# Kernel optimization log

Measured on AMD Instinct MI355X. Metric: run time of the kernel, lower is better.

The kernel has to match this reference:

```python
import jax, jax.numpy as jnp
import numpy as np

N = 100000      # nodes
E = 1000000     # edges
IN = 64         # in_dim
TD = 64         # time_dim
OUT = 64        # out_dim
H = 4           # num_heads
HD = OUT // H   # head_dim = 16


def setup_inputs() -> dict:
    key = jax.random.key(0)
    ks = jax.random.split(key, 12)
    g = lambda k, shp, s: (jax.random.normal(k, shp, jnp.float32) * s)
    return {
        "x": g(ks[0], (N, IN), 1.0),
        "time_features": g(ks[1], (N, TD), 1.0),
        "edge_index": jax.random.randint(ks[2], (2, E), 0, N, dtype=jnp.int32),
        # nn.Linear weights stored as [in, out] (already transposed)
        "q_w": g(ks[3], (IN + TD, OUT), 0.05), "q_b": g(ks[4], (OUT,), 0.05),
        "k_w": g(ks[5], (IN + TD, OUT), 0.05), "k_b": g(ks[6], (OUT,), 0.05),
        "v_w": g(ks[7], (IN, OUT), 0.05),      "v_b": g(ks[8], (OUT,), 0.05),
        "o_w": g(ks[9], (OUT, OUT), 0.05),     "o_b": g(ks[10], (OUT,), 0.05),
    }


def reference(x, time_features, edge_index, q_w, q_b, k_w, k_b, v_w, v_b, o_w, o_b):
    xt = jnp.concatenate([x, time_features], axis=-1)            # [N, IN+TD]
    Q = (xt @ q_w + q_b).reshape(N, H, HD)
    K = (xt @ k_w + k_b).reshape(N, H, HD)
    V = (x @ v_w + v_b).reshape(N, H, HD)
    src, dst = edge_index[0], edge_index[1]
    # edge-gather QK dot-product: [E, H]
    scores = jnp.sum(Q[dst] * K[src], axis=-1) / np.float32(np.sqrt(HD))
    # per-destination (segment) softmax over edges, numerically stable two-pass
    seg_max = jax.ops.segment_max(scores, dst, num_segments=N)   # [N, H]
    e = jnp.exp(scores - seg_max[dst])                           # [E, H]
    seg_sum = jax.ops.segment_sum(e, dst, num_segments=N)        # [N, H]
    attn = e / seg_sum[dst]                                      # [E, H]
    # weighted scatter-add of values
    messages = attn[..., None] * V[src]                          # [E, H, HD]
    out = jax.ops.segment_sum(messages, dst, num_segments=N)     # [N, H, HD]
    out = out.reshape(N, OUT)
    return out @ o_w + o_b
```

## Files before the change

### kernel.cpp

```cpp
#include <hip/hip_runtime.h>
#include <hip/hip_fp16.h>
#include <math.h>

#define N_NODES 100000
#define N_EDGES 1000000
#define QKV_BLOCKS ((N_NODES + 63) / 64)
#define FILL_BLOCKS ((N_EDGES + 255) / 256)
#define PREP_BLOCKS 96
#define HEAD_INT4 ((N_NODES * 8) / 4)
#define ZERO_BLOCKS ((HEAD_INT4 + 255) / 256)
#define AGG_BLOCKS (N_NODES / 16)

typedef __attribute__((ext_vector_type(8))) _Float16 f16x8;
typedef __attribute__((ext_vector_type(4))) float    f32x4;

__global__ __launch_bounds__(256) void prep_zero_kernel(
    const float* __restrict__ qw, const float* __restrict__ kw,
    const float* __restrict__ vw, const float* __restrict__ ow,
    _Float16* __restrict__ WqT, _Float16* __restrict__ WkT,
    _Float16* __restrict__ WvT, _Float16* __restrict__ WoT,
    int* __restrict__ head)
{
    if (blockIdx.x < PREP_BLOCKS) {
        const int idx = blockIdx.x * 256 + threadIdx.x;
        if (idx < 8192) {
            const int c = idx >> 7, k = idx & 127;
            WqT[idx] = (_Float16)qw[k * 64 + c];
        } else if (idx < 16384) {
            const int i = idx - 8192, c = i >> 7, k = i & 127;
            WkT[i] = (_Float16)kw[k * 64 + c];
        } else if (idx < 20480) {
            const int i = idx - 16384, c = i >> 6, k = i & 63;
            WvT[i] = (_Float16)vw[k * 64 + c];
        } else {
            const int i = idx - 20480, c = i >> 6, k = i & 63;
            WoT[i] = (_Float16)ow[k * 64 + c];
        }
    } else {
        const int idx = (blockIdx.x - PREP_BLOCKS) * 256 + threadIdx.x;
        if (idx < HEAD_INT4)
            ((int4*)head)[idx] = make_int4(-1, -1, -1, -1);
    }
}

__global__ __launch_bounds__(256) void fill_qkv_kernel(
    const int* __restrict__ src, const int* __restrict__ dst,
    int* __restrict__ head, int2* __restrict__ next2,
    const float* __restrict__ x, const float* __restrict__ tf,
    const _Float16* __restrict__ WqT, const _Float16* __restrict__ WkT,
    const _Float16* __restrict__ WvT,
    const float* __restrict__ qb, const float* __restrict__ kb,
    const float* __restrict__ vb,
    _Float16* __restrict__ Qh, _Float16* __restrict__ Kh,
    _Float16* __restrict__ Vh)
{
    __shared__ _Float16 xt[64][128];
    const int t = threadIdx.x;

    if (blockIdx.x >= QKV_BLOCKS) {
        const int e = (blockIdx.x - QKV_BLOCKS) * 256 + t;
        if (e < N_EDGES) {
            const int d  = dst[e];
            const int sv = src[e];
            const int old = atomicExch(&head[(size_t)d * 8 + (e & 7)], e);
            next2[e] = make_int2(old, sv);
        }
        return;
    }

    const int base = blockIdx.x * 64;

    {
        const int j = t & 15;
        #pragma unroll
        for (int i = 0; i < 4; ++i) {
            const int r = (t >> 4) + 16 * i;
            int node = base + r;
            if (node >= N_NODES) node = N_NODES - 1;
            const float* p = (j < 8) ? (x  + (size_t)node * 64 + 8 * j)
                                     : (tf + (size_t)node * 64 + 8 * (j - 8));
            const float4 lo = ((const float4*)p)[0];
            const float4 hi = ((const float4*)p)[1];
            f16x8 h = { (_Float16)lo.x, (_Float16)lo.y, (_Float16)lo.z,
                        (_Float16)lo.w, (_Float16)hi.x, (_Float16)hi.y,
                        (_Float16)hi.z, (_Float16)hi.w };
            const int js = j ^ (r & 15);
            *(f16x8*)&xt[r][js * 8] = h;
        }
    }

    const int wave = t >> 6;
    const int lane = t & 63;
    const int lrow = lane & 15;
    const int lgrp = lane >> 4;
    const int cw   = wave * 16;

    f16x8 bq[4], bk[4], bv[2];
    const float biasq = qb[cw + lrow];
    const float biask = kb[cw + lrow];
    const float biasv = vb[cw + lrow];
    {
        const size_t rq = (size_t)(cw + lrow) * 128 + lgrp * 8;
        #pragma unroll
        for (int kt = 0; kt < 4; ++kt) {
            bq[kt] = *(const f16x8*)&WqT[rq + kt * 32];
            bk[kt] = *(const f16x8*)&WkT[rq + kt * 32];
        }
        const size_t rv = (size_t)(cw + lrow) * 64 + lgrp * 8;
        #pragma unroll
        for (int kt = 0; kt < 2; ++kt)
            bv[kt] = *(const f16x8*)&WvT[rv + kt * 32];
    }
    __syncthreads();

    #pragma unroll
    for (int rt = 0; rt < 4; ++rt) {
        f16x8 a[4];
        const int r = rt * 16 + lrow;
        #pragma unroll
        for (int kt = 0; kt < 4; ++kt) {
            const int js = (kt * 4 + lgrp) ^ lrow;
            a[kt] = *(const f16x8*)&xt[r][js * 8];
        }
        f32x4 accq = {0.f, 0.f, 0.f, 0.f};
        f32x4 acck = {0.f, 0.f, 0.f, 0.f};
        f32x4 accv = {0.f, 0.f, 0.f, 0.f};
        #pragma unroll
        for (int kt = 0; kt < 4; ++kt) {
            accq = __builtin_amdgcn_mfma_f32_16x16x32_f16(a[kt], bq[kt], accq, 0, 0, 0);
            acck = __builtin_amdgcn_mfma_f32_16x16x32_f16(a[kt], bk[kt], acck, 0, 0, 0);
        }
        #pragma unroll
        for (int kt = 0; kt < 2; ++kt)
            accv = __builtin_amdgcn_mfma_f32_16x16x32_f16(a[kt], bv[kt], accv, 0, 0, 0);
        #pragma unroll
        for (int rr = 0; rr < 4; ++rr) {
            const int node = base + rt * 16 + lgrp * 4 + rr;
            if (node < N_NODES) {
                const size_t o = (size_t)node * 64 + cw + lrow;
                Qh[o] = (_Float16)(accq[rr] + biasq);
                Kh[o] = (_Float16)(acck[rr] + biask);
                Vh[o] = (_Float16)(accv[rr] + biasv);
            }
        }
    }
}

__global__ __launch_bounds__(256) void agg_kernel(
    const int* __restrict__ head, const int2* __restrict__ next2,
    const __half* __restrict__ Qh, const __half* __restrict__ Kh,
    const __half* __restrict__ Vh,
    const _Float16* __restrict__ WoT, const float* __restrict__ ob,
    float* __restrict__ out)
{
    __shared__ _Float16 aggh[16][64];
    const int wave = threadIdx.x >> 6;
    const int lane = threadIdx.x & 63;
    const int g    = lane >> 3;
    const int s    = lane & 7;
    const int lrow = lane & 15;
    const int lgrp = lane >> 4;
    const int nb   = blockIdx.x * 16;

    f16x8 bo0, bo1;
    {
        const size_t ro = (size_t)(wave * 16 + lrow) * 64 + lgrp * 8;
        bo0 = *(const f16x8*)&WoT[ro];
        bo1 = *(const f16x8*)&WoT[ro + 32];
    }
    const float biaso = ob[wave * 16 + lrow];

    const uint4* __restrict__ Q4 = (const uint4*)Qh;
    const uint4* __restrict__ K4 = (const uint4*)Kh;
    const uint4* __restrict__ V4 = (const uint4*)Vh;

    for (int nn = 0; nn < 4; ++nn) {
        const int node = nb + wave * 4 + nn;
        float qf[8];
        {
            const uint4 qu = Q4[(size_t)node * 8 + s];
            const __half2* qh = (const __half2*)&qu;
            #pragma unroll
            for (int j = 0; j < 4; ++j) {
                const float2 a = __half22float2(qh[j]);
                qf[2 * j] = a.x; qf[2 * j + 1] = a.y;
            }
        }

        float acc[8] = {0.f, 0.f, 0.f, 0.f, 0.f, 0.f, 0.f, 0.f};
        float ssum = 0.f;

        int e = head[(size_t)node * 8 + g];
        bool act = (e >= 0);
        while (__any(act)) {
            const int es = act ? e : 0;
            const int2 sn = next2[es];
            const int sv = sn.y;
            const uint4 ku = K4[(size_t)sv * 8 + s];
            const uint4 vu = V4[(size_t)sv * 8 + s];

            float kf[8], vf[8];
            {
                const __half2* kh = (const __half2*)&ku;
                const __half2* vh = (const __half2*)&vu;
                #pragma unroll
                for (int j = 0; j < 4; ++j) {
                    const float2 a = __half22float2(kh[j]);
                    const float2 b = __half22float2(vh[j]);
                    kf[2 * j] = a.x; kf[2 * j + 1] = a.y;
                    vf[2 * j] = b.x; vf[2 * j + 1] = b.y;
                }
            }
            float dq = qf[0] * kf[0] + qf[1] * kf[1] + qf[2] * kf[2] + qf[3] * kf[3]
                     + qf[4] * kf[4] + qf[5] * kf[5] + qf[6] * kf[6] + qf[7] * kf[7];
            dq += __shfl_xor(dq, 1);
            const float p = act ? __expf(dq * 0.25f) : 0.f;
            ssum += p;
            #pragma unroll
            for (int j = 0; j < 8; ++j) acc[j] = fmaf(p, vf[j], acc[j]);

            e = act ? sn.x : -1;
            act = (e >= 0);
        }

        #pragma unroll
        for (int m = 8; m <= 32; m <<= 1) {
            #pragma unroll
            for (int j = 0; j < 8; ++j) acc[j] += __shfl_xor(acc[j], m);
            ssum += __shfl_xor(ssum, m);
        }

        const float inv = (ssum > 0.f) ? (1.0f / ssum) : 0.0f;
        if (g == 0) {
            const int r = wave * 4 + nn;
            f16x8 h = { (_Float16)(acc[0] * inv), (_Float16)(acc[1] * inv),
                        (_Float16)(acc[2] * inv), (_Float16)(acc[3] * inv),
                        (_Float16)(acc[4] * inv), (_Float16)(acc[5] * inv),
                        (_Float16)(acc[6] * inv), (_Float16)(acc[7] * inv) };
            *(f16x8*)&aggh[r][(s ^ (r & 7)) * 8] = h;
        }
    }
    __syncthreads();

    f16x8 a0, a1;
    {
        const int p0 = (lgrp)     ^ (lrow & 7);
        const int p1 = (4 + lgrp) ^ (lrow & 7);
        a0 = *(const f16x8*)&aggh[lrow][p0 * 8];
        a1 = *(const f16x8*)&aggh[lrow][p1 * 8];
    }
    f32x4 acco = {0.f, 0.f, 0.f, 0.f};
    acco = __builtin_amdgcn_mfma_f32_16x16x32_f16(a0, bo0, acco, 0, 0, 0);
    acco = __builtin_amdgcn_mfma_f32_16x16x32_f16(a1, bo1, acco, 0, 0, 0);
    #pragma unroll
    for (int rr = 0; rr < 4; ++rr) {
        const int node = nb + lgrp * 4 + rr;
        out[(size_t)node * 64 + wave * 16 + lrow] = acco[rr] + biaso;
    }
}

extern "C" void kernel_launch(void* const* d_in, const int* in_sizes, int n_in,
                              void* d_out, int out_size, void* d_ws, size_t ws_size,
                              hipStream_t stream) {
    const float* x  = (const float*)d_in[0];
    const float* tf = (const float*)d_in[1];
    const int*   ei = (const int*)  d_in[2];
    const float* qw = (const float*)d_in[3];
    const float* qb = (const float*)d_in[4];
    const float* kw = (const float*)d_in[5];
    const float* kb = (const float*)d_in[6];
    const float* vw = (const float*)d_in[7];
    const float* vb = (const float*)d_in[8];
    const float* ow = (const float*)d_in[9];
    const float* ob = (const float*)d_in[10];
    float* out = (float*)d_out;

    char* ws = (char*)d_ws;
    const size_t hf = (size_t)N_NODES * 64 * sizeof(_Float16);

    _Float16* Qh      = (_Float16*)(ws);
    _Float16* Kh      = (_Float16*)(ws + hf);
    _Float16* Vh      = (_Float16*)(ws + 2 * hf);
    _Float16* WqT     = (_Float16*)(ws + 3 * hf);
    _Float16* WkT     = WqT + 8192;
    _Float16* WvT     = WkT + 8192;
    _Float16* WoT     = WvT + 4096;
    int*      head    = (int*)(WoT + 4096);
    int2*     next2   = (int2*)(head + (size_t)N_NODES * 8);

    const int* src = ei;
    const int* dst = ei + N_EDGES;

    const dim3 blk(256);
    prep_zero_kernel<<<dim3(PREP_BLOCKS + ZERO_BLOCKS), blk, 0, stream>>>(
        qw, kw, vw, ow, WqT, WkT, WvT, WoT, head);

    fill_qkv_kernel<<<dim3(QKV_BLOCKS + FILL_BLOCKS), blk, 0, stream>>>(
        src, dst, head, next2,
        x, tf, WqT, WkT, WvT, qb, kb, vb, Qh, Kh, Vh);

    agg_kernel<<<dim3(AGG_BLOCKS), blk, 0, stream>>>(
        head, next2, (const __half*)Qh, (const __half*)Kh, (const __half*)Vh,
        WoT, ob, out);
}
```

Baseline: 142.1 us.

## Use single linked list per node and assign one 8-lane group per node

Replaces the 8-way striped per-node edge lists with a single list head per node. The aggregation kernel now gives each 8-lane group its own destination node (32 nodes per block) rather than having a whole wave share one node with cross-group shuffle reductions. The head array is cleared with hipMemsetAsync instead of a fused zero kernel. This cuts head-array size, removes the cross-group reductions and raises node-level parallelism, at the cost of serial list chains about 8x longer per group and more wave divergence from degree imbalance.

```diff
diff --git a/kernel.cpp b/kernel.cpp
--- a/kernel.cpp
+++ b/kernel.cpp
@@ -7,39 +7,30 @@
 #define QKV_BLOCKS ((N_NODES + 63) / 64)
 #define FILL_BLOCKS ((N_EDGES + 255) / 256)
 #define PREP_BLOCKS 96
-#define HEAD_INT4 ((N_NODES * 8) / 4)
-#define ZERO_BLOCKS ((HEAD_INT4 + 255) / 256)
-#define AGG_BLOCKS (N_NODES / 16)
+#define AGG_BLOCKS (N_NODES / 32)
 
 typedef __attribute__((ext_vector_type(8))) _Float16 f16x8;
 typedef __attribute__((ext_vector_type(4))) float    f32x4;
 
-__global__ __launch_bounds__(256) void prep_zero_kernel(
+__global__ __launch_bounds__(256) void prep_kernel(
     const float* __restrict__ qw, const float* __restrict__ kw,
     const float* __restrict__ vw, const float* __restrict__ ow,
     _Float16* __restrict__ WqT, _Float16* __restrict__ WkT,
-    _Float16* __restrict__ WvT, _Float16* __restrict__ WoT,
-    int* __restrict__ head)
+    _Float16* __restrict__ WvT, _Float16* __restrict__ WoT)
 {
-    if (blockIdx.x < PREP_BLOCKS) {
-        const int idx = blockIdx.x * 256 + threadIdx.x;
-        if (idx < 8192) {
-            const int c = idx >> 7, k = idx & 127;
-            WqT[idx] = (_Float16)qw[k * 64 + c];
-        } else if (idx < 16384) {
-            const int i = idx - 8192, c = i >> 7, k = i & 127;
-            WkT[i] = (_Float16)kw[k * 64 + c];
-        } else if (idx < 20480) {
-            const int i = idx - 16384, c = i >> 6, k = i & 63;
-            WvT[i] = (_Float16)vw[k * 64 + c];
-        } else {
-            const int i = idx - 20480, c = i >> 6, k = i & 63;
-            WoT[i] = (_Float16)ow[k * 64 + c];
-        }
+    const int idx = blockIdx.x * 256 + threadIdx.x;
+    if (idx < 8192) {
+        const int c = idx >> 7, k = idx & 127;
+        WqT[idx] = (_Float16)qw[k * 64 + c];
+    } else if (idx < 16384) {
+        const int i = idx - 8192, c = i >> 7, k = i & 127;
+        WkT[i] = (_Float16)kw[k * 64 + c];
+    } else if (idx < 20480) {
+        const int i = idx - 16384, c = i >> 6, k = i & 63;
+        WvT[i] = (_Float16)vw[k * 64 + c];
     } else {
-        const int idx = (blockIdx.x - PREP_BLOCKS) * 256 + threadIdx.x;
-        if (idx < HEAD_INT4)
-            ((int4*)head)[idx] = make_int4(-1, -1, -1, -1);
+        const int i = idx - 20480, c = i >> 6, k = i & 63;
+        WoT[i] = (_Float16)ow[k * 64 + c];
     }
 }
 
@@ -62,7 +53,7 @@
         if (e < N_EDGES) {
             const int d  = dst[e];
             const int sv = src[e];
-            const int old = atomicExch(&head[(size_t)d * 8 + (e & 7)], e);
+            const int old = atomicExch(&head[d], e);
             next2[e] = make_int2(old, sv);
         }
         return;
@@ -153,109 +144,100 @@
     const _Float16* __restrict__ WoT, const float* __restrict__ ob,
     float* __restrict__ out)
 {
-    __shared__ _Float16 aggh[16][64];
+    __shared__ _Float16 aggh[32][64];
     const int wave = threadIdx.x >> 6;
     const int lane = threadIdx.x & 63;
     const int g    = lane >> 3;
     const int s    = lane & 7;
     const int lrow = lane & 15;
     const int lgrp = lane >> 4;
-    const int nb   = blockIdx.x * 16;
+    const int cw   = wave * 16;
+    const int nb   = blockIdx.x * 32;
+    const int node = nb + wave * 8 + g;
 
     f16x8 bo0, bo1;
     {
-        const size_t ro = (size_t)(wave * 16 + lrow) * 64 + lgrp * 8;
+        const size_t ro = (size_t)(cw + lrow) * 64 + lgrp * 8;
         bo0 = *(const f16x8*)&WoT[ro];
         bo1 = *(const f16x8*)&WoT[ro + 32];
     }
-    const float biaso = ob[wave * 16 + lrow];
+    const float biaso = ob[cw + lrow];
 
     const uint4* __restrict__ Q4 = (const uint4*)Qh;
     const uint4* __restrict__ K4 = (const uint4*)Kh;
     const uint4* __restrict__ V4 = (const uint4*)Vh;
 
-    for (int nn = 0; nn < 4; ++nn) {
-        const int node = nb + wave * 4 + nn;
-        float qf[8];
+    float qf[8];
+    {
+        const uint4 qu = Q4[(size_t)node * 8 + s];
+        const __half2* qh = (const __half2*)&qu;
+        #pragma unroll
+        for (int j = 0; j < 4; ++j) {
+            const float2 a = __half22float2(qh[j]);
+            qf[2 * j] = a.x; qf[2 * j + 1] = a.y;
+        }
+    }
+
+    float acc[8] = {0.f, 0.f, 0.f, 0.f, 0.f, 0.f, 0.f, 0.f};
+    float ssum = 0.f;
+
+    int e = head[node];
+    bool act = (e >= 0);
+    while (__any(act)) {
+        const int es = act ? e : 0;
+        const int2 sn = next2[es];
+        const int sv = sn.y;
+        const uint4 ku = K4[(size_t)sv * 8 + s];
+        const uint4 vu = V4[(size_t)sv * 8 + s];
+
+        float kf[8], vf[8];
         {
-            const uint4 qu = Q4[(size_t)node * 8 + s];
-            const __half2* qh = (const __half2*)&qu;
+            const __half2* kh = (const __half2*)&ku;
+            const __half2* vh = (const __half2*)&vu;
             #pragma unroll
             for (int j = 0; j < 4; ++j) {
-                const float2 a = __half22float2(qh[j]);
-                qf[2 * j] = a.x; qf[2 * j + 1] = a.y;
+                const float2 a = __half22float2(kh[j]);
+                const float2 b = __half22float2(vh[j]);
+                kf[2 * j] = a.x; kf[2 * j + 1] = a.y;
+                vf[2 * j] = b.x; vf[2 * j + 1] = b.y;
             }
         }
-
-        float acc[8] = {0.f, 0.f, 0.f, 0.f, 0.f, 0.f, 0.f, 0.f};
-        float ssum = 0.f;
-
-        int e = head[(size_t)node * 8 + g];
-        bool act = (e >= 0);
-        while (__any(act)) {
-            const int es = act ? e : 0;
-            const int2 sn = next2[es];
-            const int sv = sn.y;
-            const uint4 ku = K4[(size_t)sv * 8 + s];
-            const uint4 vu = V4[(size_t)sv * 8 + s];
-
-            float kf[8], vf[8];
-            {
-                const __half2* kh = (const __half2*)&ku;
-                const __half2* vh = (const __half2*)&vu;
-                #pragma unroll
-                for (int j = 0; j < 4; ++j) {
-                    const float2 a = __half22float2(kh[j]);
-                    const float2 b = __half22float2(vh[j]);
-                    kf[2 * j] = a.x; kf[2 * j + 1] = a.y;
-                    vf[2 * j] = b.x; vf[2 * j + 1] = b.y;
-                }
-            }
-            float dq = qf[0] * kf[0] + qf[1] * kf[1] + qf[2] * kf[2] + qf[3] * kf[3]
-                     + qf[4] * kf[4] + qf[5] * kf[5] + qf[6] * kf[6] + qf[7] * kf[7];
-            dq += __shfl_xor(dq, 1);
-            const float p = act ? __expf(dq * 0.25f) : 0.f;
-            ssum += p;
-            #pragma unroll
-            for (int j = 0; j < 8; ++j) acc[j] = fmaf(p, vf[j], acc[j]);
-
-            e = act ? sn.x : -1;
-            act = (e >= 0);
-        }
-
-        #pragma unroll
-        for (int m = 8; m <= 32; m <<= 1) {
-            #pragma unroll
-            for (int j = 0; j < 8; ++j) acc[j] += __shfl_xor(acc[j], m);
-            ssum += __shfl_xor(ssum, m);
-        }
-
+        float dq = qf[0] * kf[0] + qf[1] * kf[1] + qf[2] * kf[2] + qf[3] * kf[3]
+                 + qf[4] * kf[4] + qf[5] * kf[5] + qf[6] * kf[6] + qf[7] * kf[7];
+        dq += __shfl_xor(dq, 1);
+        const float p = act ? __expf(dq * 0.25f) : 0.f;
+        ssum += p;
+        #pragma unroll
+        for (int j = 0; j < 8; ++j) acc[j] = fmaf(p, vf[j], acc[j]);
+
+        e = act ? sn.x : -1;
+        act = (e >= 0);
+    }
+
+    {
         const float inv = (ssum > 0.f) ? (1.0f / ssum) : 0.0f;
-        if (g == 0) {
-            const int r = wave * 4 + nn;
-            f16x8 h = { (_Float16)(acc[0] * inv), (_Float16)(acc[1] * inv),
-                        (_Float16)(acc[2] * inv), (_Float16)(acc[3] * inv),
-                        (_Float16)(acc[4] * inv), (_Float16)(acc[5] * inv),
-                        (_Float16)(acc[6] * inv), (_Float16)(acc[7] * inv) };
-            *(f16x8*)&aggh[r][(s ^ (r & 7)) * 8] = h;
-        }
+        const int r = wave * 8 + g;
+        f16x8 h = { (_Float16)(acc[0] * inv), (_Float16)(acc[1] * inv),
+                    (_Float16)(acc[2] * inv), (_Float16)(acc[3] * inv),
+                    (_Float16)(acc[4] * inv), (_Float16)(acc[5] * inv),
+                    (_Float16)(acc[6] * inv), (_Float16)(acc[7] * inv) };
+        *(f16x8*)&aggh[r][(s ^ g) * 8] = h;
     }
     __syncthreads();
 
-    f16x8 a0, a1;
-    {
-        const int p0 = (lgrp)     ^ (lrow & 7);
-        const int p1 = (4 + lgrp) ^ (lrow & 7);
-        a0 = *(const f16x8*)&aggh[lrow][p0 * 8];
-        a1 = *(const f16x8*)&aggh[lrow][p1 * 8];
-    }
-    f32x4 acco = {0.f, 0.f, 0.f, 0.f};
-    acco = __builtin_amdgcn_mfma_f32_16x16x32_f16(a0, bo0, acco, 0, 0, 0);
-    acco = __builtin_amdgcn_mfma_f32_16x16x32_f16(a1, bo1, acco, 0, 0, 0);
     #pragma unroll
-    for (int rr = 0; rr < 4; ++rr) {
-        const int node = nb + lgrp * 4 + rr;
-        out[(size_t)node * 64 + wave * 16 + lrow] = acco[rr] + biaso;
+    for (int rt = 0; rt < 2; ++rt) {
+        const int r = rt * 16 + lrow;
+        f16x8 a0 = *(const f16x8*)&aggh[r][((lgrp)     ^ (lrow & 7)) * 8];
+        f16x8 a1 = *(const f16x8*)&aggh[r][((4 + lgrp) ^ (lrow & 7)) * 8];
+        f32x4 acco = {0.f, 0.f, 0.f, 0.f};
+        acco = __builtin_amdgcn_mfma_f32_16x16x32_f16(a0, bo0, acco, 0, 0, 0);
+        acco = __builtin_amdgcn_mfma_f32_16x16x32_f16(a1, bo1, acco, 0, 0, 0);
+        #pragma unroll
+        for (int rr = 0; rr < 4; ++rr) {
+            const int n = nb + rt * 16 + lgrp * 4 + rr;
+            out[(size_t)n * 64 + cw + lrow] = acco[rr] + biaso;
+        }
     }
 }
 
@@ -286,14 +268,17 @@
     _Float16* WvT     = WkT + 8192;
     _Float16* WoT     = WvT + 4096;
     int*      head    = (int*)(WoT + 4096);
-    int2*     next2   = (int2*)(head + (size_t)N_NODES * 8);
+    int2*     next2   = (int2*)(head + N_NODES);
 
     const int* src = ei;
     const int* dst = ei + N_EDGES;
 
     const dim3 blk(256);
-    prep_zero_kernel<<<dim3(PREP_BLOCKS + ZERO_BLOCKS), blk, 0, stream>>>(
-        qw, kw, vw, ow, WqT, WkT, WvT, WoT, head);
+
+    hipMemsetAsync(head, 0xFF, N_NODES * sizeof(int), stream);
+
+    prep_kernel<<<dim3(PREP_BLOCKS), blk, 0, stream>>>(
+        qw, kw, vw, ow, WqT, WkT, WvT, WoT);
 
     fill_qkv_kernel<<<dim3(QKV_BLOCKS + FILL_BLOCKS), blk, 0, stream>>>(
         src, dst, head, next2,
```

New measurement: 140.9 us. No clear change (-0.9%).
